# Optimization experiments

Hardware: AMD Instinct MI355X
Metric: run time of the kernel (lower is better)

## Reference

```python
import jax, jax.numpy as jnp
import numpy as np

N = 4096            # data_length
T_IN, D_IN = 64, 128
F = 32 * 64         # target_length * output_dim


def setup_inputs() -> dict:
    key = jax.random.key(0)
    k1, k2, k3, k4 = jax.random.split(key, 4)
    xs = jax.random.normal(k1, (N, T_IN, D_IN), dtype=jnp.float32)
    W = jax.random.normal(k2, (T_IN * D_IN, F), dtype=jnp.float32) / np.sqrt(T_IN * D_IN)
    ys = jax.random.randint(k3, (N,), 0, 2, dtype=jnp.int32)  # {0,1} -> mapped to +-1 labels
    alphas = jax.random.normal(k4, (N,), dtype=jnp.float32)
    return {"xs": xs, "W": W, "ys": ys, "alphas": alphas}


def reference(xs, W, ys, alphas):
    gamma = 1.0 / F  # RBF bandwidth
    # encoder (stand-in for seq2seq): [N, T*D] @ [T*D, F] -> [N, F]
    X = xs.reshape(N, -1) @ W
    # pairwise squared distances via gram trick
    sq = jnp.sum(X * X, axis=-1)                       # [N]
    d2 = sq[:, None] + sq[None, :] - 2.0 * (X @ X.T)   # [N, N]
    d2 = jnp.maximum(d2, 0.0)
    K = jnp.exp(-gamma * d2)                           # RBF kernel matrix
    lab = (2 * ys - 1).astype(X.dtype)                 # +-1 labels
    G = (lab[:, None] * lab[None, :]) * K              # gram[i][j] = y_i y_j k(x_i, x_j)
    # 0.5 * alpha^T G alpha - sum(alpha)
    value = 0.5 * jnp.dot(alphas, G @ alphas) - jnp.sum(alphas)
    return value.reshape(1, 1)
```

## Files before the change

kernel.cpp:

```cpp
#include <hip/hip_runtime.h>
#include <hip/hip_bf16.h>

#define N_ROWS 4096
#define K_IN   8192
#define F_DIM  2048
#define GAMMA  (1.0f / 2048.0f)

typedef unsigned short u16;
typedef unsigned int   u32;
typedef unsigned char  u8;
typedef __attribute__((ext_vector_type(4))) int   i32x4;
typedef __attribute__((ext_vector_type(8))) int   i32x8;
typedef __attribute__((ext_vector_type(4))) float f32x4;
typedef __attribute__((ext_vector_type(2))) float f32x2;

__device__ __forceinline__ u32 pk4_fp8(float a, float b, float c, float d) {
  u32 u = 0;
  u = __builtin_amdgcn_cvt_pk_fp8_f32(a, b, u, false);
  u = __builtin_amdgcn_cvt_pk_fp8_f32(c, d, u, true);
  return u;
}
__device__ __forceinline__ u8 f8(float v) {
  return (u8)(__builtin_amdgcn_cvt_pk_fp8_f32(v, v, 0, false) & 0xff);
}

__device__ __forceinline__ void async16(const void* g, void* l) {
  __builtin_amdgcn_global_load_lds(
      (const __attribute__((address_space(1))) void*)g,
      (__attribute__((address_space(3))) void*)l, 16, 0, 0);
}


__global__ void convert_xs(const float4* __restrict__ in, u32* __restrict__ out, int n4) {
  int base = blockIdx.x * (blockDim.x * 4) + threadIdx.x;
#pragma unroll
  for (int k = 0; k < 4; ++k) {
    int i = base + k * 256;
    if (i < n4) {
      float4 v = in[i];
      out[i] = pk4_fp8(v.x, v.y, v.z, v.w);
    }
  }
}

__global__ void transpose_w(const float* __restrict__ W, u8* __restrict__ Wt) {
  __shared__ float tile[128][33];
  int k0 = blockIdx.x * 128;
  int f0 = blockIdx.y * 32;
  int tx = threadIdx.x, ty = threadIdx.y;
#pragma unroll
  for (int kk = 0; kk < 16; ++kk) {
    int k = kk * 8 + ty;
    tile[k][tx] = 64.0f * W[(size_t)(k0 + k) * F_DIM + f0 + tx];
  }
  __syncthreads();
#pragma unroll
  for (int ff = 0; ff < 4; ++ff) {
    int f = ff * 8 + ty;
    int kk = tx * 4;
    u32 p = pk4_fp8(tile[kk][f], tile[kk + 1][f], tile[kk + 2][f], tile[kk + 3][f]);
    *(u32*)(Wt + (size_t)(f0 + f) * K_IN + k0 + kk) = p;
  }
}

__global__ void prep(const float* __restrict__ alphas, const int* __restrict__ ys,
                     float* __restrict__ beta, float* __restrict__ out) {
  __shared__ float red[1024];
  int t = threadIdx.x;
  float s = 0.f;
  for (int i = t; i < N_ROWS; i += 1024) {
    float a = alphas[i];
    beta[i] = a * (float)(2 * ys[i] - 1);
    s += a;
  }
  red[t] = s;
  __syncthreads();
  for (int off = 512; off; off >>= 1) {
    if (t < off) red[t] += red[t + off];
    __syncthreads();
  }
  if (t == 0) out[0] = -red[0];
}

__global__ void row_sq(const u32* __restrict__ X, float* __restrict__ sq) {
  int wave = threadIdx.x >> 6, lane = threadIdx.x & 63;
  int row = blockIdx.x * 4 + wave;
  const uint4* xr = (const uint4*)(X + (size_t)row * (F_DIM / 4));
  float s = 0.f;
#pragma unroll
  for (int it = 0; it < 2; ++it) {
    uint4 v = xr[lane + it * 64];
    u32 w[4] = {v.x, v.y, v.z, v.w};
#pragma unroll
    for (int p = 0; p < 4; ++p) {
      f32x2 lo = __builtin_amdgcn_cvt_pk_f32_fp8(w[p], false);
      f32x2 hi = __builtin_amdgcn_cvt_pk_f32_fp8(w[p], true);
      s += lo[0] * lo[0] + lo[1] * lo[1] + hi[0] * hi[0] + hi[1] * hi[1];
    }
  }
#pragma unroll
  for (int off = 32; off; off >>= 1) s += __shfl_down(s, off);
  if (lane == 0) sq[row] = s;
}


template <int K>
__device__ __forceinline__ void gemm_tile_f8(const u8* __restrict__ A, const u8* __restrict__ Bt,
                                             int m0, int n0, u8* sA, u8* sB, int tid,
                                             int sclA, int sclB, f32x4 acc[4][4]) {
  const int lane = tid & 63;
  const int q = lane >> 4;
  const int r = lane & 15;
  const int wave = tid >> 6;
  const int wm = (wave >> 1) << 6;
  const int wn = (wave & 1) << 6;

  const f32x4 zero = {0.f, 0.f, 0.f, 0.f};
#pragma unroll
  for (int mt = 0; mt < 4; ++mt)
#pragma unroll
    for (int nt = 0; nt < 4; ++nt) acc[mt][nt] = zero;

  int rowS[4], colS[4], offS[4];
#pragma unroll
  for (int j = 0; j < 4; ++j) {
    int o = tid * 16 + j * 4096;
    int row = o >> 7;
    int cb = (o >> 4) & 7;
    rowS[j] = row;
    colS[j] = ((cb ^ (row & 7)) << 4);
    offS[j] = o;
  }

  for (int k0 = 0; k0 < K; k0 += 128) {
#pragma unroll
    for (int j = 0; j < 4; ++j) {
      async16(A + (size_t)(m0 + rowS[j]) * K + k0 + colS[j], sA + offS[j]);
      async16(Bt + (size_t)(n0 + rowS[j]) * K + k0 + colS[j], sB + offS[j]);
    }
    __syncthreads();

    i32x8 af[4], bg[4];
#pragma unroll
    for (int mt = 0; mt < 4; ++mt) {
      int m = wm + (mt << 4) + r;
      i32x4 lo = *(const i32x4*)(sA + m * 128 + ((((q << 1) | 0) ^ (m & 7)) << 4));
      i32x4 hi = *(const i32x4*)(sA + m * 128 + ((((q << 1) | 1) ^ (m & 7)) << 4));
      i32x8 f = {lo[0], lo[1], lo[2], lo[3], hi[0], hi[1], hi[2], hi[3]};
      af[mt] = f;
    }
#pragma unroll
    for (int nt = 0; nt < 4; ++nt) {
      int n = wn + (nt << 4) + r;
      i32x4 lo = *(const i32x4*)(sB + n * 128 + ((((q << 1) | 0) ^ (n & 7)) << 4));
      i32x4 hi = *(const i32x4*)(sB + n * 128 + ((((q << 1) | 1) ^ (n & 7)) << 4));
      i32x8 f = {lo[0], lo[1], lo[2], lo[3], hi[0], hi[1], hi[2], hi[3]};
      bg[nt] = f;
    }
#pragma unroll
    for (int mt = 0; mt < 4; ++mt)
#pragma unroll
      for (int nt = 0; nt < 4; ++nt)
        acc[mt][nt] = __builtin_amdgcn_mfma_scale_f32_16x16x128_f8f6f4(
            af[mt], bg[nt], acc[mt][nt], 0, 0, 0, sclA, 0, sclB);
    __syncthreads();
  }
}

__global__ __launch_bounds__(256, 3) void gemm_xw(const u8* __restrict__ A,
                                                  const u8* __restrict__ Bt,
                                                  u8* __restrict__ X) {
  __shared__ __align__(16) u8 sA[128 * 128];
  __shared__ __align__(16) u8 sB[128 * 128];
  const int tid = threadIdx.x;
  const int m0 = blockIdx.y << 7;
  const int n0 = blockIdx.x << 7;
  f32x4 acc[4][4];
  gemm_tile_f8<K_IN>(A, Bt, m0, n0, sA, sB, tid, 127, 121, acc);

  const int lane = tid & 63;
  const int q = lane >> 4;
  const int r = lane & 15;
  const int wave = tid >> 6;
  const int wm = (wave >> 1) << 6;
  const int wn = (wave & 1) << 6;
#pragma unroll
  for (int mt = 0; mt < 4; ++mt) {
#pragma unroll
    for (int nt = 0; nt < 4; ++nt) {
      int row = m0 + wm + (mt << 4) + (q << 2);
      int col = n0 + wn + (nt << 4) + r;
#pragma unroll
      for (int e = 0; e < 4; ++e)
        X[(size_t)(row + e) * F_DIM + col] = f8(acc[mt][nt][e]);
    }
  }
}

__global__ __launch_bounds__(256, 3) void gemm_kern(const u8* __restrict__ X,
                                                    const float* __restrict__ sq,
                                                    const float* __restrict__ beta,
                                                    float* __restrict__ out) {
  __shared__ __align__(16) u8 sA[128 * 128];
  __shared__ __align__(16) u8 sB[128 * 128];
  const int tid = threadIdx.x;
  int bid = blockIdx.x;
  int ib = 0;
  while (bid >= 32 - ib) { bid -= 32 - ib; ++ib; }
  const int jb = ib + bid;
  const int m0 = ib << 7;
  const int n0 = jb << 7;

  f32x4 acc[4][4];
  gemm_tile_f8<F_DIM>(X, X, m0, n0, sA, sB, tid, 127, 127, acc);

  const int lane = tid & 63;
  const int q = lane >> 4;
  const int r = lane & 15;
  const int wave = tid >> 6;
  const int wm = (wave >> 1) << 6;
  const int wn = (wave & 1) << 6;

  float sqj[4], bj[4];
#pragma unroll
  for (int nt = 0; nt < 4; ++nt) {
    int j = n0 + wn + (nt << 4) + r;
    sqj[nt] = sq[j];
    bj[nt] = beta[j];
  }
  float local = 0.f;
#pragma unroll
  for (int mt = 0; mt < 4; ++mt) {
#pragma unroll
    for (int e = 0; e < 4; ++e) {
      int i = m0 + wm + (mt << 4) + (q << 2) + e;
      float sqi = sq[i];
      float bi = beta[i];
#pragma unroll
      for (int nt = 0; nt < 4; ++nt) {
        float d2 = fmaxf(sqi + sqj[nt] - 2.f * acc[mt][nt][e], 0.f);
        local += bi * bj[nt] * __expf(-GAMMA * d2);
      }
    }
  }
  local *= (ib == jb) ? 0.5f : 1.0f;
#pragma unroll
  for (int off = 32; off; off >>= 1) local += __shfl_down(local, off);
  if (lane == 0) atomicAdd(out, local);
}


extern "C" void kernel_launch(void* const* d_in, const int* in_sizes, int n_in,
                              void* d_out, int out_size, void* d_ws, size_t ws_size,
                              hipStream_t stream) {
  const float* xs = (const float*)d_in[0];
  const float* W = (const float*)d_in[1];
  const int* ys = (const int*)d_in[2];
  const float* alphas = (const float*)d_in[3];
  float* out = (float*)d_out;

  char* ws = (char*)d_ws;
  u8* xs_f8 = (u8*)ws;
  u8* Wt_f8 = (u8*)(ws + 33554432);
  u8* X_f8  = (u8*)(ws + 50331648);
  float* sq   = (float*)(ws + 58720256);
  float* beta = (float*)(ws + 58736640);

  convert_xs<<<8192, 256, 0, stream>>>((const float4*)xs, (u32*)xs_f8,
                                       (N_ROWS * K_IN) / 4);
  dim3 tb(32, 8);
  dim3 tg(K_IN / 128, F_DIM / 32);
  transpose_w<<<tg, tb, 0, stream>>>(W, Wt_f8);
  prep<<<1, 1024, 0, stream>>>(alphas, ys, beta, out);

  dim3 g1(F_DIM / 128, N_ROWS / 128);
  gemm_xw<<<g1, 256, 0, stream>>>(xs_f8, Wt_f8, X_f8);
  row_sq<<<N_ROWS / 4, 256, 0, stream>>>((const u32*)X_f8, sq);
  gemm_kern<<<528, 256, 0, stream>>>(X_f8, sq, beta, out);
}
```

Before: 366.9 us.

## Fuse prep kernels into one launch and compute row norms in GEMM epilogue

Merges the xs conversion, W transpose/quantization and alpha/label prep into one block-indexed kernel. The row_sq kernel is dropped: the XW GEMM epilogue decodes each stored fp8 value, accumulates its square, reduces across lanes and atomically adds into sq, which the prep kernel zeroes. This removes three launches and a re-read of X, at the cost of float atomics (nondeterministic summation order) and a larger epilogue.

```diff
diff --git a/kernel.cpp b/kernel.cpp
--- a/kernel.cpp
+++ b/kernel.cpp
@@ -23,6 +23,10 @@
 __device__ __forceinline__ u8 f8(float v) {
   return (u8)(__builtin_amdgcn_cvt_pk_fp8_f32(v, v, 0, false) & 0xff);
 }
+__device__ __forceinline__ float f8_dec(u8 b) {
+  f32x2 d = __builtin_amdgcn_cvt_pk_f32_fp8((u32)b, false);
+  return d[0];
+}
 
 __device__ __forceinline__ void async16(const void* g, void* l) {
   __builtin_amdgcn_global_load_lds(
@@ -30,77 +34,58 @@
       (__attribute__((address_space(3))) void*)l, 16, 0, 0);
 }
 
-
-__global__ void convert_xs(const float4* __restrict__ in, u32* __restrict__ out, int n4) {
-  int base = blockIdx.x * (blockDim.x * 4) + threadIdx.x;
-#pragma unroll
-  for (int k = 0; k < 4; ++k) {
-    int i = base + k * 256;
-    if (i < n4) {
-      float4 v = in[i];
-      out[i] = pk4_fp8(v.x, v.y, v.z, v.w);
-    }
-  }
-}
-
-__global__ void transpose_w(const float* __restrict__ W, u8* __restrict__ Wt) {
+__global__ __launch_bounds__(256) void fused_prep(
+    const float4* __restrict__ xs4, u32* __restrict__ xs_f8,
+    const float* __restrict__ W, u8* __restrict__ Wt,
+    const float* __restrict__ alphas, const int* __restrict__ ys,
+    float* __restrict__ beta, float* __restrict__ sq, float* __restrict__ out) {
   __shared__ float tile[128][33];
-  int k0 = blockIdx.x * 128;
-  int f0 = blockIdx.y * 32;
-  int tx = threadIdx.x, ty = threadIdx.y;
-#pragma unroll
-  for (int kk = 0; kk < 16; ++kk) {
-    int k = kk * 8 + ty;
-    tile[k][tx] = 64.0f * W[(size_t)(k0 + k) * F_DIM + f0 + tx];
-  }
-  __syncthreads();
-#pragma unroll
-  for (int ff = 0; ff < 4; ++ff) {
-    int f = ff * 8 + ty;
-    int kk = tx * 4;
-    u32 p = pk4_fp8(tile[kk][f], tile[kk + 1][f], tile[kk + 2][f], tile[kk + 3][f]);
-    *(u32*)(Wt + (size_t)(f0 + f) * K_IN + k0 + kk) = p;
-  }
-}
-
-__global__ void prep(const float* __restrict__ alphas, const int* __restrict__ ys,
-                     float* __restrict__ beta, float* __restrict__ out) {
-  __shared__ float red[1024];
-  int t = threadIdx.x;
-  float s = 0.f;
-  for (int i = t; i < N_ROWS; i += 1024) {
-    float a = alphas[i];
-    beta[i] = a * (float)(2 * ys[i] - 1);
-    s += a;
-  }
-  red[t] = s;
-  __syncthreads();
-  for (int off = 512; off; off >>= 1) {
-    if (t < off) red[t] += red[t + off];
-    __syncthreads();
-  }
-  if (t == 0) out[0] = -red[0];
-}
-
-__global__ void row_sq(const u32* __restrict__ X, float* __restrict__ sq) {
-  int wave = threadIdx.x >> 6, lane = threadIdx.x & 63;
-  int row = blockIdx.x * 4 + wave;
-  const uint4* xr = (const uint4*)(X + (size_t)row * (F_DIM / 4));
-  float s = 0.f;
-#pragma unroll
-  for (int it = 0; it < 2; ++it) {
-    uint4 v = xr[lane + it * 64];
-    u32 w[4] = {v.x, v.y, v.z, v.w};
-#pragma unroll
-    for (int p = 0; p < 4; ++p) {
-      f32x2 lo = __builtin_amdgcn_cvt_pk_f32_fp8(w[p], false);
-      f32x2 hi = __builtin_amdgcn_cvt_pk_f32_fp8(w[p], true);
-      s += lo[0] * lo[0] + lo[1] * lo[1] + hi[0] * hi[0] + hi[1] * hi[1];
-    }
-  }
-#pragma unroll
-  for (int off = 32; off; off >>= 1) s += __shfl_down(s, off);
-  if (lane == 0) sq[row] = s;
+  __shared__ float red[256];
+  const int bid = blockIdx.x;
+  const int tid = threadIdx.x;
+
+  if (bid < 8192) {
+    int base = bid * 1024 + tid;
+#pragma unroll
+    for (int k = 0; k < 4; ++k) {
+      int i = base + k * 256;
+      float4 v = xs4[i];
+      xs_f8[i] = pk4_fp8(v.x, v.y, v.z, v.w);
+    }
+  } else if (bid < 12288) {
+    int t = bid - 8192;
+    int k0 = (t & 63) * 128;
+    int f0 = (t >> 6) * 32;
+    int tx = tid & 31, ty = tid >> 5;
+#pragma unroll
+    for (int kk = 0; kk < 16; ++kk) {
+      int k = kk * 8 + ty;
+      tile[k][tx] = 64.0f * W[(size_t)(k0 + k) * F_DIM + f0 + tx];
+    }
+    __syncthreads();
+#pragma unroll
+    for (int ff = 0; ff < 4; ++ff) {
+      int f = ff * 8 + ty;
+      int kk = tx * 4;
+      u32 p = pk4_fp8(tile[kk][f], tile[kk + 1][f], tile[kk + 2][f], tile[kk + 3][f]);
+      *(u32*)(Wt + (size_t)(f0 + f) * K_IN + k0 + kk) = p;
+    }
+  } else {
+    float s = 0.f;
+    for (int i = tid; i < N_ROWS; i += 256) {
+      float a = alphas[i];
+      beta[i] = a * (float)(2 * ys[i] - 1);
+      sq[i] = 0.f;
+      s += a;
+    }
+    red[tid] = s;
+    __syncthreads();
+    for (int off = 128; off; off >>= 1) {
+      if (tid < off) red[tid] += red[tid + off];
+      __syncthreads();
+    }
+    if (tid == 0) out[0] = -red[0];
+  }
 }
 
 
@@ -169,7 +154,8 @@
 
 __global__ __launch_bounds__(256, 3) void gemm_xw(const u8* __restrict__ A,
                                                   const u8* __restrict__ Bt,
-                                                  u8* __restrict__ X) {
+                                                  u8* __restrict__ X,
+                                                  float* __restrict__ sq) {
   __shared__ __align__(16) u8 sA[128 * 128];
   __shared__ __align__(16) u8 sB[128 * 128];
   const int tid = threadIdx.x;
@@ -184,6 +170,13 @@
   const int wave = tid >> 6;
   const int wm = (wave >> 1) << 6;
   const int wn = (wave & 1) << 6;
+
+  float sqs[4][4];
+#pragma unroll
+  for (int mt = 0; mt < 4; ++mt)
+#pragma unroll
+    for (int e = 0; e < 4; ++e) sqs[mt][e] = 0.f;
+
 #pragma unroll
   for (int mt = 0; mt < 4; ++mt) {
 #pragma unroll
@@ -191,8 +184,22 @@
       int row = m0 + wm + (mt << 4) + (q << 2);
       int col = n0 + wn + (nt << 4) + r;
 #pragma unroll
-      for (int e = 0; e < 4; ++e)
-        X[(size_t)(row + e) * F_DIM + col] = f8(acc[mt][nt][e]);
+      for (int e = 0; e < 4; ++e) {
+        u8 b = f8(acc[mt][nt][e]);
+        X[(size_t)(row + e) * F_DIM + col] = b;
+        float xd = f8_dec(b);
+        sqs[mt][e] += xd * xd;
+      }
+    }
+  }
+#pragma unroll
+  for (int mt = 0; mt < 4; ++mt) {
+#pragma unroll
+    for (int e = 0; e < 4; ++e) {
+      float s = sqs[mt][e];
+#pragma unroll
+      for (int off = 8; off; off >>= 1) s += __shfl_down(s, off);
+      if (r == 0) atomicAdd(&sq[m0 + wm + (mt << 4) + (q << 2) + e], s);
     }
   }
 }
@@ -266,15 +273,10 @@
   float* sq   = (float*)(ws + 58720256);
   float* beta = (float*)(ws + 58736640);
 
-  convert_xs<<<8192, 256, 0, stream>>>((const float4*)xs, (u32*)xs_f8,
-                                       (N_ROWS * K_IN) / 4);
-  dim3 tb(32, 8);
-  dim3 tg(K_IN / 128, F_DIM / 32);
-  transpose_w<<<tg, tb, 0, stream>>>(W, Wt_f8);
-  prep<<<1, 1024, 0, stream>>>(alphas, ys, beta, out);
+  fused_prep<<<12289, 256, 0, stream>>>((const float4*)xs, (u32*)xs_f8,
+                                        W, Wt_f8, alphas, ys, beta, sq, out);
 
   dim3 g1(F_DIM / 128, N_ROWS / 128);
-  gemm_xw<<<g1, 256, 0, stream>>>(xs_f8, Wt_f8, X_f8);
-  row_sq<<<N_ROWS / 4, 256, 0, stream>>>((const u32*)X_f8, sq);
+  gemm_xw<<<g1, 256, 0, stream>>>(xs_f8, Wt_f8, X_f8, sq);
   gemm_kern<<<528, 256, 0, stream>>>(X_f8, sq, beta, out);
 }
```

New measurement: 368.9 us. No clear change (+0.5%).
